# Kernel tuning notes

Measured on AMD Instinct MI355X. Metric: run time of the kernel, lower is better.

Reference implementation:

```python
import jax, jax.numpy as jnp
import numpy as np

T = 5          # temporal_window_size
B = 512        # batch (graphs per timestep)
NA = 16        # num_agents (nodes per graph)
S = 64         # num_belief_states
A = 16         # action_dim
HID = 64       # hidden_dim per head
H = 4          # num_attn_heads
FD = HID * H   # 256, feature_dim
LAT = 128      # latent_dim
N = B * NA     # total nodes per timestep
FIN = S + A    # node feature dim
NEG_SLOPE = 0.2


def _edge_index():
    i, j = np.meshgrid(np.arange(NA), np.arange(NA), indexing='ij')
    m = i != j
    src_l, dst_l = i[m], j[m]                      # 240 intra-clique edges
    off = (np.arange(B) * NA)[:, None]
    src = (src_l[None] + off).ravel()
    dst = (dst_l[None] + off).ravel()
    loops = np.arange(N)                           # PyG GATConv add_self_loops=True
    src = np.concatenate([src, loops])
    dst = np.concatenate([dst, loops])
    return jnp.asarray(np.stack([src, dst]), dtype=jnp.int64)


def setup_inputs() -> dict:
    key = jax.random.key(0)
    ks = jax.random.split(key, 24)
    xav = lambda k, shp: jax.random.normal(k, shp, jnp.float32) * np.float32(np.sqrt(2.0 / (shp[0] + shp[-1])))
    return {
        'signals': jax.random.normal(ks[0], (T, B, S), jnp.float32),
        'neighbor_actions': jax.random.normal(ks[1], (T, B, NA * A), jnp.float32),
        'lin_w0': xav(ks[2], (FD, FIN)),
        'att_src0': xav(ks[3], (H, HID)),
        'att_dst0': xav(ks[4], (H, HID)),
        'bias0': jnp.zeros((FD,), jnp.float32),
        'lin_w1': xav(ks[5], (FD, FD)),
        'att_src1': xav(ks[6], (H, HID)),
        'att_dst1': xav(ks[7], (H, HID)),
        'bias1': jnp.zeros((FD,), jnp.float32),
        'in_proj_w': xav(ks[8], (3 * FD, FD)),
        'in_proj_b': jnp.zeros((3 * FD,), jnp.float32),
        'out_proj_w': xav(ks[9], (FD, FD)),
        'out_proj_b': jnp.zeros((FD,), jnp.float32),
        'w_mean': xav(ks[10], (LAT, FD)),
        'b_mean': jnp.zeros((LAT,), jnp.float32),
        'w_logvar': xav(ks[11], (LAT, FD)),
        'b_logvar': jnp.zeros((LAT,), jnp.float32),
        'w_belief': xav(ks[12], (S, FD)),
        'b_belief': jnp.zeros((S,), jnp.float32),
        'edge_index': _edge_index(),
    }


def _segment_softmax(e, seg, num_segments):
    # e: [E, T, H]; softmax over edges sharing the same target node.
    m = jax.ops.segment_max(e, seg, num_segments=num_segments)
    e = jnp.exp(e - m[seg])
    s = jax.ops.segment_sum(e, seg, num_segments=num_segments)
    return e / s[seg]


def _gat(x, src, dst, w, a_src, a_dst, b):
    # x: [N, T, Fin] -> [N, T, H*HID]   (PyG GATConv, concat heads)
    xl = jnp.einsum('ntf,of->nto', x, w).reshape(N, T, H, HID)
    e_src = jnp.einsum('nthc,hc->nth', xl, a_src)[src]   # [E, T, H]
    e_dst = jnp.einsum('nthc,hc->nth', xl, a_dst)[dst]
    e = jax.nn.leaky_relu(e_src + e_dst, NEG_SLOPE)
    alpha = _segment_softmax(e, dst, N)                  # per-target softmax
    out = jax.ops.segment_sum(alpha[..., None] * xl[src], dst, num_segments=N)
    return out.reshape(N, T, FD) + b


def reference(signals, neighbor_actions, lin_w0, att_src0, att_dst0, bias0,
              lin_w1, att_src1, att_dst1, bias1, in_proj_w, in_proj_b,
              out_proj_w, out_proj_b, w_mean, b_mean, w_logvar, b_logvar,
              w_belief, b_belief, edge_index):
    # --- _construct_graph (vectorized over time window + batch) ---
    acts = neighbor_actions.reshape(T, B, NA, A)
    beliefs = jnp.zeros((T, B, NA, S), signals.dtype).at[:, :, 0, :].set(signals)
    nodes = jnp.concatenate([beliefs, acts], -1).reshape(T, N, FIN)
    nodes = jnp.transpose(nodes, (1, 0, 2))              # [N, T, FIN]
    src, dst = edge_index[0], edge_index[1]
    x = jax.nn.relu(_gat(nodes, src, dst, lin_w0, att_src0, att_dst0, bias0))
    x = jax.nn.relu(_gat(x, src, dst, lin_w1, att_src1, att_dst1, bias1))
    # --- ego-node sequence: nodes 0, NA, 2*NA, ... ---
    seq = x[::NA]                                        # [B, T, FD]
    # --- temporal MultiheadAttention (batch_first, eval) ---
    qkv = seq @ in_proj_w.T + in_proj_b
    q, k, v = jnp.split(qkv, 3, axis=-1)
    dh = FD // H
    q = q.reshape(B, T, H, dh); k = k.reshape(B, T, H, dh); v = v.reshape(B, T, H, dh)
    scores = jnp.einsum('bqhd,bkhd->bhqk', q, k) / jnp.sqrt(jnp.asarray(dh, seq.dtype))
    # torch float attn_mask is ADDITIVE: mask[i,j]=1 if j<=i else 0
    mask = (jnp.arange(T)[:, None] >= jnp.arange(T)[None, :]).astype(seq.dtype)
    attn = jax.nn.softmax(scores + mask[None, None], axis=-1)
    ctx = jnp.einsum('bhqk,bkhd->bqhd', attn, v).reshape(B, T, FD)
    ctx = ctx @ out_proj_w.T + out_proj_b
    feat = ctx[:, -1]                                    # [B, FD]
    # --- heads ---
    mean = feat @ w_mean.T + b_mean
    logvar = feat @ w_logvar.T + b_logvar
    belief = jax.nn.softmax(feat @ w_belief.T + b_belief, axis=-1)
    return (mean, logvar, belief)
```

## Files before the change

kernel.cpp:

```cpp
#include <hip/hip_runtime.h>
#include <hip/hip_bf16.h>


__device__ __forceinline__ float wave_sum64(float v) {
    #pragma unroll
    for (int off = 32; off > 0; off >>= 1) v += __shfl_xor(v, off, 64);
    return v;
}
__device__ __forceinline__ float wave_max64(float v) {
    #pragma unroll
    for (int off = 32; off > 0; off >>= 1) v = fmaxf(v, __shfl_xor(v, off, 64));
    return v;
}

__global__ __launch_bounds__(256) void k_pre(
    const float* __restrict__ w0, const float* __restrict__ w1,
    const float* __restrict__ wip, const float* __restrict__ wop,
    const float* __restrict__ wm, const float* __restrict__ wlv,
    const float* __restrict__ wb,
    const float* __restrict__ as0, const float* __restrict__ ad0,
    const float* __restrict__ as1, const float* __restrict__ ad1,
    float* __restrict__ tws,
    float* __restrict__ u1, float* __restrict__ ud1,
    float* __restrict__ pa0, float* __restrict__ pd0)
{
    const int tid = threadIdx.x;
    if (blockIdx.x < 1680) {
        int i = blockIdx.x * 256 + tid;
        float v;
        if (i < 16384) {
            int k = i >> 8, n = i & 255;
            v = w0[n * 80 + k];
        } else if (i < 20480) {
            int j = i - 16384; int k = j >> 8, n = j & 255;
            v = w0[n * 80 + 64 + k];
        } else if (i < 86016) {
            int j = i - 20480; int k = j >> 8, n = j & 255;
            v = w1[n * 256 + k];
        } else if (i < 282624) {
            int j = i - 86016; int k = j / 768, n = j - k * 768;
            v = wip[n * 256 + k];
        } else if (i < 348160) {
            int j = i - 282624; int k = j >> 8, n = j & 255;
            v = wop[n * 256 + k];
        } else {
            int j = i - 348160; int k = j / 320, o = j - k * 320;
            if (o < 128)      v = wm[o * 256 + k];
            else if (o < 256) v = wlv[(o - 128) * 256 + k];
            else              v = wb[(o - 256) * 256 + k];
        }
        tws[i] = v;
        return;
    }
    for (int q = 0; q < 4; q++) {
        int idx = q * 256 + tid;
        int h = idx >> 8, k = idx & 255;
        float su = 0.f, sd = 0.f;
        for (int c = 0; c < 64; c++) {
            float wv = w1[(h * 64 + c) * 256 + k];
            su = fmaf(as1[h * 64 + c], wv, su);
            sd = fmaf(ad1[h * 64 + c], wv, sd);
        }
        u1[idx] = su; ud1[idx] = sd;
    }
    if (tid < 64) {
        int h = tid >> 4, k = tid & 15;
        float su = 0.f, sd = 0.f;
        for (int c = 0; c < 64; c++) {
            float wv = w0[(h * 64 + c) * 80 + 64 + k];
            su = fmaf(as0[h * 64 + c], wv, su);
            sd = fmaf(ad0[h * 64 + c], wv, sd);
        }
        pa0[tid] = su; pd0[tid] = sd;
    }
}

__global__ __launch_bounds__(256) void k_gat(
    const float* __restrict__ sig,
    const float* __restrict__ nact,
    const float* __restrict__ W0sT,
    const float* __restrict__ W0aT,
    const float* __restrict__ W1T,
    const float* __restrict__ u1g, const float* __restrict__ ud1g,
    const float* __restrict__ pa0g, const float* __restrict__ pd0g,
    const float* __restrict__ as0, const float* __restrict__ ad0,
    const float* __restrict__ b0, const float* __restrict__ b1,
    float* __restrict__ seqf)
{
    __shared__ __align__(16) char smem[36832];
    float* actL   = (float*)(smem + 0);
    float* u1L    = (float*)(smem + 1024);
    float* ud1L   = (float*)(smem + 5136);
    float* pa0L   = (float*)(smem + 9248);
    float* pd0L   = (float*)(smem + 9504);
    float* sSL    = (float*)(smem + 9760);
    float* dSL    = (float*)(smem + 9776);
    float* es0L   = (float*)(smem + 9792);
    float* ed0L   = (float*)(smem + 10048);
    float* a0L    = (float*)(smem + 10304);
    float* dLa    = (float*)(smem + 14400);
    float* zLa    = (float*)(smem + 14400);
    float* x1L    = (float*)(smem + 18512);
    float* espL   = (float*)(smem + 34960);
    float* edpL   = (float*)(smem + 35984);
    float* es1L   = (float*)(smem + 36048);
    float* edLx   = (float*)(smem + 36304);
    float* alpha1L= (float*)(smem + 36320);
    float* sigL   = (float*)(smem + 36576);

    const int tid = threadIdx.x;
    const int bg = blockIdx.x;
    const int b = bg / 5, g = bg - b * 5;
    const int n = tid, w = tid >> 6, lane = tid & 63;

    if (tid < 64) sigL[tid] = sig[(g * 512 + b) * 64 + tid];
    actL[tid] = nact[(g * 512 + b) * 256 + tid];
    #pragma unroll
    for (int q = 0; q < 4; q++) {
        int idx = q * 256 + tid;
        int h = idx >> 8, k = idx & 255;
        u1L[h * 257 + k] = u1g[idx];
        ud1L[h * 257 + k] = ud1g[idx];
    }
    if (tid >= 64 && tid < 128) { pa0L[tid - 64] = pa0g[tid - 64]; pd0L[tid - 64] = pd0g[tid - 64]; }
    __syncthreads();

    float S = 0.f;
    for (int k = 0; k < 64; k++)
        S = fmaf(sigL[k], W0sT[k * 256 + n], S);
    {
        float ps = wave_sum64(S * as0[n]);
        float pd_ = wave_sum64(S * ad0[n]);
        if (lane == 0) { sSL[w] = ps; dSL[w] = pd_; }
    }
    __syncthreads();

    if (tid < 64) {
        int m = tid >> 2, h = tid & 3;
        float su = (m == 0) ? sSL[h] : 0.f;
        float sd = (m == 0) ? dSL[h] : 0.f;
        #pragma unroll
        for (int k = 0; k < 16; k++) {
            float av = actL[m * 16 + k];
            su = fmaf(av, pa0L[h * 16 + k], su);
            sd = fmaf(av, pd0L[h * 16 + k], sd);
        }
        es0L[m * 4 + h] = su; ed0L[m * 4 + h] = sd;
    }
    __syncthreads();

    if (tid < 64) {
        int h = tid >> 4, j = tid & 15;
        float ej = ed0L[j * 4 + h];
        float e[16], m = -1e30f;
        #pragma unroll
        for (int s = 0; s < 16; s++) {
            float x = es0L[s * 4 + h] + ej;
            x = (x >= 0.f) ? x : 0.2f * x;
            e[s] = x; m = fmaxf(m, x);
        }
        float sum = 0.f;
        #pragma unroll
        for (int s = 0; s < 16; s++) { e[s] = __expf(e[s] - m); sum += e[s]; }
        float inv = 1.f / sum;
        #pragma unroll
        for (int s = 0; s < 16; s++) a0L[h * 256 + j * 16 + s] = e[s] * inv;
    }
    __syncthreads();

    #pragma unroll
    for (int q = 0; q < 4; q++) {
        int idx = q * 256 + tid;
        int h = idx >> 8, j = (idx >> 4) & 15, k = idx & 15;
        float a = 0.f;
        #pragma unroll
        for (int s = 0; s < 16; s++)
            a = fmaf(a0L[h * 256 + j * 16 + s], actL[s * 16 + k], a);
        dLa[h * 256 + j * 16 + k] = a;
    }
    __syncthreads();

    float x1r[16];
    {
        const int h = w;
        float b0v = b0[n];
        #pragma unroll
        for (int j = 0; j < 16; j++)
            x1r[j] = fmaf(a0L[h * 256 + j * 16], S, b0v);
        #pragma unroll
        for (int k = 0; k < 16; k++) {
            float wv = W0aT[k * 256 + n];
            #pragma unroll
            for (int j = 0; j < 16; j++)
                x1r[j] = fmaf(dLa[h * 256 + j * 16 + k], wv, x1r[j]);
        }
        #pragma unroll
        for (int j = 0; j < 16; j++) {
            x1r[j] = fmaxf(x1r[j], 0.f);
            x1L[j * 257 + n] = x1r[j];
        }
    }
    __syncthreads();

    {
        int m = tid >> 4, h = (tid >> 2) & 3, p = tid & 3;
        float a = 0.f;
        for (int kk = 0; kk < 64; kk++) {
            int k = kk * 4 + p;
            a = fmaf(x1L[m * 257 + k], u1L[h * 257 + k], a);
        }
        espL[m * 16 + h * 4 + p] = a;
        if (m == 0) {
            float ad = 0.f;
            for (int kk = 0; kk < 64; kk++) {
                int k = kk * 4 + p;
                ad = fmaf(x1L[k], ud1L[h * 257 + k], ad);
            }
            edpL[h * 4 + p] = ad;
        }
    }
    __syncthreads();
    if (tid < 64) {
        int m = tid >> 2, h = tid & 3;
        const float* e = espL + m * 16 + h * 4;
        es1L[m * 4 + h] = e[0] + e[1] + e[2] + e[3];
    }
    if (tid < 4)
        edLx[tid] = edpL[tid * 4] + edpL[tid * 4 + 1] + edpL[tid * 4 + 2] + edpL[tid * 4 + 3];
    __syncthreads();

    if (tid < 4) {
        int h = tid;
        float ej = edLx[h];
        float e[16], m = -1e30f;
        #pragma unroll
        for (int s = 0; s < 16; s++) {
            float x = es1L[s * 4 + h] + ej;
            x = (x >= 0.f) ? x : 0.2f * x;
            e[s] = x; m = fmaxf(m, x);
        }
        float sum = 0.f;
        #pragma unroll
        for (int s = 0; s < 16; s++) { e[s] = __expf(e[s] - m); sum += e[s]; }
        float inv = 1.f / sum;
        #pragma unroll
        for (int s = 0; s < 16; s++) alpha1L[h * 16 + s] = e[s] * inv;
    }
    __syncthreads();

    {
        const int k = tid;
        float xv[16];
        #pragma unroll
        for (int s = 0; s < 16; s++) xv[s] = x1L[s * 257 + k];
        #pragma unroll
        for (int h = 0; h < 4; h++) {
            float zv = 0.f;
            #pragma unroll
            for (int s = 0; s < 16; s++)
                zv = fmaf(alpha1L[h * 16 + s], xv[s], zv);
            zLa[h * 257 + k] = zv;
        }
    }
    __syncthreads();

    {
        const int h = w;
        float acc = b1[n];
        for (int k = 0; k < 256; k++)
            acc = fmaf(zLa[h * 257 + k], W1T[k * 256 + n], acc);
        seqf[bg * 256 + n] = fmaxf(acc, 0.f);
    }
}

__global__ __launch_bounds__(768) void k_stage2(
    const float* __restrict__ seqf,
    const float* __restrict__ wipT,
    const float* __restrict__ bip,
    const float* __restrict__ wopT,
    const float* __restrict__ bop,
    const float* __restrict__ whT,
    const float* __restrict__ bm, const float* __restrict__ blv,
    const float* __restrict__ bb,
    float* __restrict__ out)
{
    __shared__ float sseq[2][5][256];
    __shared__ float kL[2][5][256], vL[2][5][256], qL[2][256];
    __shared__ float ctxL[2][256], featL[2][256];
    __shared__ float beliefL[2][64];
    const int tid = threadIdx.x;
    const int b0 = blockIdx.x * 2;

    {
        float* sflat = &sseq[0][0][0];
        for (int i = tid; i < 2560; i += 768)
            sflat[i] = seqf[b0 * 1280 + i];
    }
    __syncthreads();

    {
        const int kind = tid >> 8, n = tid & 255;
        if (kind == 0) {
            float a0 = 0.f, a1 = 0.f;
            for (int k = 0; k < 256; k++) {
                float wv = wipT[k * 768 + n];
                a0 = fmaf(sseq[0][4][k], wv, a0);
                a1 = fmaf(sseq[1][4][k], wv, a1);
            }
            float bv = bip[n];
            qL[0][n] = a0 + bv; qL[1][n] = a1 + bv;
        } else {
            const float* wcol = wipT + kind * 256 + n;
            float acc[2][5];
            #pragma unroll
            for (int gb = 0; gb < 2; gb++)
                #pragma unroll
                for (int t = 0; t < 5; t++) acc[gb][t] = 0.f;
            for (int k = 0; k < 256; k++) {
                float wv = wcol[k * 768];
                #pragma unroll
                for (int gb = 0; gb < 2; gb++) {
                    #pragma unroll
                    for (int t = 0; t < 5; t++)
                        acc[gb][t] = fmaf(sseq[gb][t][k], wv, acc[gb][t]);
                }
            }
            float bv = bip[kind * 256 + n];
            float* dst = (kind == 1) ? &kL[0][0][0] : &vL[0][0][0];
            #pragma unroll
            for (int gb = 0; gb < 2; gb++)
                #pragma unroll
                for (int t = 0; t < 5; t++)
                    dst[gb * 1280 + t * 256 + n] = acc[gb][t] + bv;
        }
    }
    __syncthreads();

    if (tid < 512) {
        const int gb = tid >> 8, col = tid & 255;
        float q4 = qL[gb][col];
        float sc[5];
        #pragma unroll
        for (int t = 0; t < 5; t++)
            sc[t] = wave_sum64(q4 * kL[gb][t][col]) * 0.125f;
        float m = sc[0];
        #pragma unroll
        for (int t = 1; t < 5; t++) m = fmaxf(m, sc[t]);
        float p[5], sum = 0.f;
        #pragma unroll
        for (int t = 0; t < 5; t++) { p[t] = __expf(sc[t] - m); sum += p[t]; }
        float inv = 1.f / sum, cv = 0.f;
        #pragma unroll
        for (int t = 0; t < 5; t++) cv = fmaf(p[t], vL[gb][t][col], cv);
        ctxL[gb][col] = cv * inv;
    }
    __syncthreads();

    if (tid < 512) {
        const int gb = tid >> 8, n = tid & 255;
        float acc = 0.f;
        for (int k = 0; k < 256; k++)
            acc = fmaf(ctxL[gb][k], wopT[k * 256 + n], acc);
        featL[gb][n] = acc + bop[n];
    }
    __syncthreads();

    if (tid < 640) {
        const int gb = tid / 320, j = tid - gb * 320;
        float acc = 0.f;
        for (int k = 0; k < 256; k++)
            acc = fmaf(featL[gb][k], whT[k * 320 + j], acc);
        if (j < 128) {
            out[(b0 + gb) * 128 + j] = acc + bm[j];
        } else if (j < 256) {
            out[65536 + (b0 + gb) * 128 + (j - 128)] = acc + blv[j - 128];
        } else {
            beliefL[gb][j - 256] = acc + bb[j - 256];
        }
    }
    __syncthreads();

    if (tid < 128) {
        int gb = tid >> 6, lane = tid & 63;
        float lg = beliefL[gb][lane];
        float m = wave_max64(lg);
        float e = __expf(lg - m);
        float s = wave_sum64(e);
        out[131072 + (b0 + gb) * 64 + lane] = e / s;
    }
}

extern "C" void kernel_launch(void* const* d_in, const int* in_sizes, int n_in,
                              void* d_out, int out_size, void* d_ws, size_t ws_size,
                              hipStream_t stream) {
    const float* sig  = (const float*)d_in[0];
    const float* nact = (const float*)d_in[1];
    const float* w0   = (const float*)d_in[2];
    const float* as0  = (const float*)d_in[3];
    const float* ad0  = (const float*)d_in[4];
    const float* b0   = (const float*)d_in[5];
    const float* w1   = (const float*)d_in[6];
    const float* as1  = (const float*)d_in[7];
    const float* ad1  = (const float*)d_in[8];
    const float* b1   = (const float*)d_in[9];
    const float* wip  = (const float*)d_in[10];
    const float* bip  = (const float*)d_in[11];
    const float* wop  = (const float*)d_in[12];
    const float* bop  = (const float*)d_in[13];
    const float* wm   = (const float*)d_in[14];
    const float* bm   = (const float*)d_in[15];
    const float* wlv  = (const float*)d_in[16];
    const float* blv  = (const float*)d_in[17];
    const float* wb   = (const float*)d_in[18];
    const float* bb   = (const float*)d_in[19];

    float* ws    = (float*)d_ws;
    float* seqf  = ws;
    float* tws   = ws + 655360;
    float* W0sT  = tws;
    float* W0aT  = tws + 16384;
    float* W1T   = tws + 20480;
    float* wipT  = tws + 86016;
    float* wopT  = tws + 282624;
    float* whT   = tws + 348160;
    float* u1    = ws + 1085440;
    float* ud1   = ws + 1086464;
    float* pa0   = ws + 1087488;
    float* pd0   = ws + 1087552;

    k_pre   <<<1681, 256, 0, stream>>>(w0, w1, wip, wop, wm, wlv, wb,
                                       as0, ad0, as1, ad1,
                                       tws, u1, ud1, pa0, pd0);
    k_gat   <<<2560, 256, 0, stream>>>(sig, nact, W0sT, W0aT, W1T,
                                       u1, ud1, pa0, pd0, as0, ad0, b0, b1, seqf);
    k_stage2<<<256, 768, 0, stream>>>(seqf, wipT, bip, wopT, bop, whT,
                                      bm, blv, bb, (float*)d_out);
}
```

Baseline: 204.6 us.

## Reorder GAT layer-0 aggregation, vectorize LDS reads, keep x1 in registers

Layer-0 output is now computed by first projecting each source node's action features through W0a (per thread column) and then aggregating with attention weights. This replaces the old aggregate-actions-then-project path and drops one LDS pass plus a barrier. The layer-1 aggregation reuses the x1 values already held in registers instead of re-reading them from LDS. LDS rows are padded to 260 floats so dot products and weight loops can use float4 reads. This trades a little more register pressure for fewer LDS transactions and synchronisations.

```diff
diff --git a/kernel.cpp b/kernel.cpp
--- a/kernel.cpp
+++ b/kernel.cpp
@@ -87,26 +87,25 @@
     const float* __restrict__ b0, const float* __restrict__ b1,
     float* __restrict__ seqf)
 {
-    __shared__ __align__(16) char smem[36832];
-    float* actL   = (float*)(smem + 0);
-    float* u1L    = (float*)(smem + 1024);
-    float* ud1L   = (float*)(smem + 5136);
-    float* pa0L   = (float*)(smem + 9248);
-    float* pd0L   = (float*)(smem + 9504);
-    float* sSL    = (float*)(smem + 9760);
-    float* dSL    = (float*)(smem + 9776);
-    float* es0L   = (float*)(smem + 9792);
-    float* ed0L   = (float*)(smem + 10048);
-    float* a0L    = (float*)(smem + 10304);
-    float* dLa    = (float*)(smem + 14400);
-    float* zLa    = (float*)(smem + 14400);
-    float* x1L    = (float*)(smem + 18512);
-    float* espL   = (float*)(smem + 34960);
-    float* edpL   = (float*)(smem + 35984);
-    float* es1L   = (float*)(smem + 36048);
-    float* edLx   = (float*)(smem + 36304);
-    float* alpha1L= (float*)(smem + 36320);
-    float* sigL   = (float*)(smem + 36576);
+    __shared__ __align__(16) char smem[37168];
+    float* actL    = (float*)(smem + 0);
+    float* sigL    = (float*)(smem + 1024);
+    float* u1L     = (float*)(smem + 1280);
+    float* ud1L    = (float*)(smem + 5440);
+    float* pa0L    = (float*)(smem + 9600);
+    float* pd0L    = (float*)(smem + 9856);
+    float* sSL     = (float*)(smem + 10112);
+    float* dSL     = (float*)(smem + 10128);
+    float* es0L    = (float*)(smem + 10144);
+    float* ed0L    = (float*)(smem + 10400);
+    float* espL    = (float*)(smem + 10656);
+    float* es1L    = (float*)(smem + 11680);
+    float* edpL    = (float*)(smem + 11936);
+    float* edL     = (float*)(smem + 12000);
+    float* alpha1L = (float*)(smem + 12016);
+    float* a0L     = (float*)(smem + 12272);
+    float* zL      = (float*)(smem + 16368);
+    float* x1L     = (float*)(smem + 20528);
 
     const int tid = threadIdx.x;
     const int bg = blockIdx.x;
@@ -119,16 +118,26 @@
     for (int q = 0; q < 4; q++) {
         int idx = q * 256 + tid;
         int h = idx >> 8, k = idx & 255;
-        u1L[h * 257 + k] = u1g[idx];
-        ud1L[h * 257 + k] = ud1g[idx];
-    }
-    if (tid >= 64 && tid < 128) { pa0L[tid - 64] = pa0g[tid - 64]; pd0L[tid - 64] = pd0g[tid - 64]; }
+        u1L[h * 260 + k] = u1g[idx];
+        ud1L[h * 260 + k] = ud1g[idx];
+    }
+    if (tid >= 64 && tid < 128) {
+        pa0L[tid - 64] = pa0g[tid - 64];
+        pd0L[tid - 64] = pd0g[tid - 64];
+    }
     __syncthreads();
 
     float S = 0.f;
-    for (int k = 0; k < 64; k++)
-        S = fmaf(sigL[k], W0sT[k * 256 + n], S);
-    {
+    {
+        const float4* sig4 = (const float4*)sigL;
+        #pragma unroll 4
+        for (int i = 0; i < 16; i++) {
+            float4 sv = sig4[i];
+            S = fmaf(sv.x, W0sT[(i * 4 + 0) * 256 + n], S);
+            S = fmaf(sv.y, W0sT[(i * 4 + 1) * 256 + n], S);
+            S = fmaf(sv.z, W0sT[(i * 4 + 2) * 256 + n], S);
+            S = fmaf(sv.w, W0sT[(i * 4 + 3) * 256 + n], S);
+        }
         float ps = wave_sum64(S * as0[n]);
         float pd_ = wave_sum64(S * ad0[n]);
         if (lane == 0) { sSL[w] = ps; dSL[w] = pd_; }
@@ -163,58 +172,79 @@
         #pragma unroll
         for (int s = 0; s < 16; s++) { e[s] = __expf(e[s] - m); sum += e[s]; }
         float inv = 1.f / sum;
-        #pragma unroll
-        for (int s = 0; s < 16; s++) a0L[h * 256 + j * 16 + s] = e[s] * inv;
-    }
-    __syncthreads();
-
-    #pragma unroll
-    for (int q = 0; q < 4; q++) {
-        int idx = q * 256 + tid;
-        int h = idx >> 8, j = (idx >> 4) & 15, k = idx & 15;
+        float4* a04 = (float4*)(a0L + h * 256 + j * 16);
+        #pragma unroll
+        for (int s4 = 0; s4 < 4; s4++)
+            a04[s4] = make_float4(e[s4 * 4] * inv, e[s4 * 4 + 1] * inv,
+                                  e[s4 * 4 + 2] * inv, e[s4 * 4 + 3] * inv);
+    }
+    __syncthreads();
+
+    float x1r[16];
+    {
+        const int h = w;
+        float wr[16];
+        #pragma unroll
+        for (int k = 0; k < 16; k++) wr[k] = W0aT[k * 256 + n];
+        const float4* act4 = (const float4*)actL;
+        float xl0r[16];
+        #pragma unroll
+        for (int s = 0; s < 16; s++) {
+            float a = 0.f;
+            #pragma unroll
+            for (int q = 0; q < 4; q++) {
+                float4 av = act4[s * 4 + q];
+                a = fmaf(av.x, wr[q * 4 + 0], a);
+                a = fmaf(av.y, wr[q * 4 + 1], a);
+                a = fmaf(av.z, wr[q * 4 + 2], a);
+                a = fmaf(av.w, wr[q * 4 + 3], a);
+            }
+            xl0r[s] = a;
+        }
+        xl0r[0] += S;
+        const float b0v = b0[n];
+        const float4* a04 = (const float4*)(a0L + h * 256);
+        #pragma unroll
+        for (int j = 0; j < 16; j++) {
+            float acc = b0v;
+            #pragma unroll
+            for (int s4 = 0; s4 < 4; s4++) {
+                float4 a4 = a04[j * 4 + s4];
+                acc = fmaf(a4.x, xl0r[s4 * 4 + 0], acc);
+                acc = fmaf(a4.y, xl0r[s4 * 4 + 1], acc);
+                acc = fmaf(a4.z, xl0r[s4 * 4 + 2], acc);
+                acc = fmaf(a4.w, xl0r[s4 * 4 + 3], acc);
+            }
+            x1r[j] = fmaxf(acc, 0.f);
+            x1L[j * 260 + n] = x1r[j];
+        }
+    }
+    __syncthreads();
+
+    {
+        const int m = tid & 15, h = (tid >> 4) & 3, p = tid >> 6;
+        const float4* x4p = (const float4*)(x1L + m * 260 + p * 64);
+        const float4* u4p = (const float4*)(u1L + h * 260 + p * 64);
         float a = 0.f;
         #pragma unroll
-        for (int s = 0; s < 16; s++)
-            a = fmaf(a0L[h * 256 + j * 16 + s], actL[s * 16 + k], a);
-        dLa[h * 256 + j * 16 + k] = a;
-    }
-    __syncthreads();
-
-    float x1r[16];
-    {
-        const int h = w;
-        float b0v = b0[n];
-        #pragma unroll
-        for (int j = 0; j < 16; j++)
-            x1r[j] = fmaf(a0L[h * 256 + j * 16], S, b0v);
-        #pragma unroll
-        for (int k = 0; k < 16; k++) {
-            float wv = W0aT[k * 256 + n];
-            #pragma unroll
-            for (int j = 0; j < 16; j++)
-                x1r[j] = fmaf(dLa[h * 256 + j * 16 + k], wv, x1r[j]);
-        }
-        #pragma unroll
-        for (int j = 0; j < 16; j++) {
-            x1r[j] = fmaxf(x1r[j], 0.f);
-            x1L[j * 257 + n] = x1r[j];
-        }
-    }
-    __syncthreads();
-
-    {
-        int m = tid >> 4, h = (tid >> 2) & 3, p = tid & 3;
-        float a = 0.f;
-        for (int kk = 0; kk < 64; kk++) {
-            int k = kk * 4 + p;
-            a = fmaf(x1L[m * 257 + k], u1L[h * 257 + k], a);
+        for (int i = 0; i < 16; i++) {
+            float4 xv = x4p[i], uv = u4p[i];
+            a = fmaf(xv.x, uv.x, a);
+            a = fmaf(xv.y, uv.y, a);
+            a = fmaf(xv.z, uv.z, a);
+            a = fmaf(xv.w, uv.w, a);
         }
         espL[m * 16 + h * 4 + p] = a;
         if (m == 0) {
+            const float4* ud4p = (const float4*)(ud1L + h * 260 + p * 64);
             float ad = 0.f;
-            for (int kk = 0; kk < 64; kk++) {
-                int k = kk * 4 + p;
-                ad = fmaf(x1L[k], ud1L[h * 257 + k], ad);
+            #pragma unroll
+            for (int i = 0; i < 16; i++) {
+                float4 xv = x4p[i], uv = ud4p[i];
+                ad = fmaf(xv.x, uv.x, ad);
+                ad = fmaf(xv.y, uv.y, ad);
+                ad = fmaf(xv.z, uv.z, ad);
+                ad = fmaf(xv.w, uv.w, ad);
             }
             edpL[h * 4 + p] = ad;
         }
@@ -226,12 +256,12 @@
         es1L[m * 4 + h] = e[0] + e[1] + e[2] + e[3];
     }
     if (tid < 4)
-        edLx[tid] = edpL[tid * 4] + edpL[tid * 4 + 1] + edpL[tid * 4 + 2] + edpL[tid * 4 + 3];
+        edL[tid] = edpL[tid * 4] + edpL[tid * 4 + 1] + edpL[tid * 4 + 2] + edpL[tid * 4 + 3];
     __syncthreads();
 
     if (tid < 4) {
         int h = tid;
-        float ej = edLx[h];
+        float ej = edL[h];
         float e[16], m = -1e30f;
         #pragma unroll
         for (int s = 0; s < 16; s++) {
@@ -249,26 +279,34 @@
     __syncthreads();
 
     {
-        const int k = tid;
-        float xv[16];
-        #pragma unroll
-        for (int s = 0; s < 16; s++) xv[s] = x1L[s * 257 + k];
-        #pragma unroll
-        for (int h = 0; h < 4; h++) {
+        const float4* a14 = (const float4*)alpha1L;
+        #pragma unroll
+        for (int hh = 0; hh < 4; hh++) {
             float zv = 0.f;
             #pragma unroll
-            for (int s = 0; s < 16; s++)
-                zv = fmaf(alpha1L[h * 16 + s], xv[s], zv);
-            zLa[h * 257 + k] = zv;
-        }
-    }
-    __syncthreads();
-
-    {
-        const int h = w;
+            for (int s4 = 0; s4 < 4; s4++) {
+                float4 a4 = a14[hh * 4 + s4];
+                zv = fmaf(a4.x, x1r[s4 * 4 + 0], zv);
+                zv = fmaf(a4.y, x1r[s4 * 4 + 1], zv);
+                zv = fmaf(a4.z, x1r[s4 * 4 + 2], zv);
+                zv = fmaf(a4.w, x1r[s4 * 4 + 3], zv);
+            }
+            zL[hh * 260 + n] = zv;
+        }
+    }
+    __syncthreads();
+
+    {
+        const float4* zh = (const float4*)(zL + w * 260);
         float acc = b1[n];
-        for (int k = 0; k < 256; k++)
-            acc = fmaf(zLa[h * 257 + k], W1T[k * 256 + n], acc);
+        #pragma unroll 8
+        for (int i = 0; i < 64; i++) {
+            float4 z4 = zh[i];
+            acc = fmaf(z4.x, W1T[(i * 4 + 0) * 256 + n], acc);
+            acc = fmaf(z4.y, W1T[(i * 4 + 1) * 256 + n], acc);
+            acc = fmaf(z4.z, W1T[(i * 4 + 2) * 256 + n], acc);
+            acc = fmaf(z4.w, W1T[(i * 4 + 3) * 256 + n], acc);
+        }
         seqf[bg * 256 + n] = fmaxf(acc, 0.f);
     }
 }
```

After: 201.2 us. No clear change (-1.6%).
